# Optimization experiments

Measured on AMD Instinct MI355X. Metric: run time of the kernel, lower is better.

Reference implementation:

```python
import jax, jax.numpy as jnp
import numpy as np

EPS = 1e-4

def mp_weight(w):
    # MP_GeoLinear eval-mode weight: normalize then scale by gain/sqrt(fan_in)
    w32 = w.astype(jnp.float32)
    norm = jnp.linalg.norm(w32, axis=1, keepdims=True)          # [out,1]
    fan_in = w.shape[1]
    denom = EPS + norm / np.sqrt(fan_in)                        # torch.add(eps, norm, alpha=sqrt(1/fan_in))
    wn = w32 / denom
    return (wn / np.sqrt(fan_in)).astype(w.dtype)               # gain=1


def setup_inputs() -> dict:
    key = jax.random.key(0)
    k1, k2, k3, k4 = jax.random.split(key, 4)
    N, E, C = 100000, 1600000, 128
    x = jax.random.normal(k1, (N, C), dtype=jnp.float32)
    edge_index = jax.random.randint(k2, (2, E), 0, N, dtype=jnp.int64)
    w_neigh = jax.random.normal(k3, (C, C), dtype=jnp.float32)
    w_res = jax.random.normal(k4, (C, C), dtype=jnp.float32)
    return {"x": x, "edge_index": edge_index, "w_neigh": w_neigh, "w_res": w_res}


def reference(x, edge_index, w_neigh, w_res):
    N = x.shape[0]
    row, col = edge_index[0], edge_index[1]            # source, target
    # degree of target nodes
    deg = jax.ops.segment_sum(jnp.ones_like(col, dtype=x.dtype), col, num_segments=N)
    deg_inv = jnp.where(deg > 0, deg ** -0.5, 0.0)     # inf -> 0
    norm = deg_inv[col]                                 # [E]
    # message: x_j * norm, aggregate: scatter-add into col
    msg = x[row] * norm[:, None]                        # [E,C]
    agg = jax.ops.segment_sum(msg, col, num_segments=N) # [N,C]
    neighbourhood = agg @ mp_weight(w_neigh).T
    residual = x @ mp_weight(w_res).T
    # mp_sum(residual, neighbourhood, t=0.5) = (a+b)/sqrt(2)
    join = (residual + neighbourhood) / np.sqrt(2.0)
    out = jnp.where((deg > 0)[:, None], join, residual)
    return out
```

## Files before the change

kernel.cpp:

```cpp
#include <hip/hip_runtime.h>
#include <hip/hip_bf16.h>

#define C 128
#define INV_SQRT2 0.7071067811865476f
#define NB 1024
#define BS 128
#define EPB 16384
#define CAPB 2560
#define LIDX_CAP 3456
#define AGS 68
#define GSTRIDE 16

typedef __attribute__((ext_vector_type(8))) short short8;
typedef __attribute__((ext_vector_type(4))) float f32x4;

__device__ inline ushort f2b(float f) {
    __hip_bfloat16 h = __float2bfloat16(f);
    return __builtin_bit_cast(ushort, h);
}


__global__ __launch_bounds__(512) void k_front(
    const int* __restrict__ row, const int* __restrict__ col, int E, int nblk,
    int* __restrict__ gcursor, unsigned int* __restrict__ recs,
    const float4* __restrict__ x, ushort* __restrict__ xb, int n4, int castBlocks,
    const float* __restrict__ w_res, const float* __restrict__ w_neigh,
    ushort* __restrict__ Bp)
{
    __shared__ int hist[NB];
    __shared__ int lbase[NB];
    int b = blockIdx.x;
    int t = threadIdx.x;
    if (b < nblk) {
        hist[t] = 0; hist[t + 512] = 0;
        __syncthreads();
        int base = b * EPB;
        #pragma unroll 4
        for (int i = 0; i < EPB / 512; i++) {
            int e = base + i * 512 + t;
            if (e < E) atomicAdd(&hist[col[e] >> 7], 1);
        }
        __syncthreads();
        #pragma unroll
        for (int kx = 0; kx < 2; kx++) {
            int bb = t + kx * 512;
            int h = hist[bb];
            lbase[bb] = h ? atomicAdd(&gcursor[bb * GSTRIDE], h) : 0;
        }
        __syncthreads();
        hist[t] = 0; hist[t + 512] = 0;
        __syncthreads();
        #pragma unroll 4
        for (int i = 0; i < EPB / 512; i++) {
            int e = base + i * 512 + t;
            if (e < E) {
                int c = col[e];
                int kk = c >> 7;
                int p = atomicAdd(&hist[kk], 1) + lbase[kk];
                if (p < CAPB)
                    recs[(size_t)kk * CAPB + p] =
                        ((unsigned int)(c & 127) << 24) | (unsigned int)row[e];
            }
        }
    } else if (b < nblk + castBlocks) {
        int i = (b - nblk) * 512 + t;
        if (i < n4) {
            float4 v = x[i];
            ushort4 o;
            o.x = f2b(v.x); o.y = f2b(v.y); o.z = f2b(v.z); o.w = f2b(v.w);
            *(ushort4*)(xb + (size_t)i * 4) = o;
        }
        if (b == nblk && t < 32) {
            ushort4 z = make_ushort4(0, 0, 0, 0);
            *(ushort4*)(xb + ((size_t)n4 << 2) + (t << 2)) = z;
        }
    } else {
        int r = (b - nblk - castBlocks) * 8 + (t >> 6);
        int h = r >> 7;
        int i = r & 127;
        const float* w = h ? w_neigh : w_res;
        int lane = t & 63;
        float a = w[i * C + lane];
        float bb = w[i * C + lane + 64];
        float ss = a * a + bb * bb;
        #pragma unroll
        for (int off = 32; off > 0; off >>= 1) ss += __shfl_down(ss, off);
        ss = __shfl(ss, 0);
        float norm = sqrtf(ss);
        float denom = 1e-4f + norm * 0.08838834764831845f;
        float scale = 1.0f / (denom * 11.313708498984761f);
        int c1 = lane, c2 = lane + 64;
        Bp[(size_t)(h * 16 + (c1 >> 3)) * 1024 + i * 8 + (c1 & 7)] = f2b(a * scale);
        Bp[(size_t)(h * 16 + (c2 >> 3)) * 1024 + i * 8 + (c2 & 7)] = f2b(bb * scale);
    }
}


#define ACCUM(v) do { \
    acc[0] += __builtin_bit_cast(float, (v).x << 16); \
    acc[1] += __builtin_bit_cast(float, (v).x & 0xffff0000u); \
    acc[2] += __builtin_bit_cast(float, (v).y << 16); \
    acc[3] += __builtin_bit_cast(float, (v).y & 0xffff0000u); \
    acc[4] += __builtin_bit_cast(float, (v).z << 16); \
    acc[5] += __builtin_bit_cast(float, (v).z & 0xffff0000u); \
    acc[6] += __builtin_bit_cast(float, (v).w << 16); \
    acc[7] += __builtin_bit_cast(float, (v).w & 0xffff0000u); \
} while (0)

__global__ __launch_bounds__(512, 8) void k_fused(
    const unsigned int* __restrict__ recs, const int* __restrict__ gcursor,
    const ushort* __restrict__ xb, const ushort* __restrict__ Bp,
    int* __restrict__ lidxg, float* __restrict__ out, int N)
{
    __shared__ int shist[BS];
    __shared__ int sexcl[BS];
    __shared__ int scur[BS];
    __shared__ uint sAgg[BS * AGS];

    int k = blockIdx.x;
    int t = threadIdx.x;
    int cnt = gcursor[k * GSTRIDE];
    if (cnt > CAPB) cnt = CAPB;
    const unsigned int* rb = recs + (size_t)k * CAPB;
    int* lw = lidxg + (size_t)k * LIDX_CAP;

    if (t < BS) shist[t] = 0;
    __syncthreads();
    for (int i = t; i < cnt; i += 512)
        atomicAdd(&shist[rb[i] >> 24], 1);
    __syncthreads();
    if (t < 64) {
        int a = shist[t], b = shist[t + 64];
        int pa = (a + 7) & ~7, pb = (b + 7) & ~7;
        int ia = pa, ib = pb;
        #pragma unroll
        for (int off = 1; off < 64; off <<= 1) {
            int ya = __shfl_up(ia, off);
            int yb = __shfl_up(ib, off);
            if (t >= off) { ia += ya; ib += yb; }
        }
        int tot0 = __shfl(ia, 63);
        int e0 = ia - pa;
        int e1 = ib - pb + tot0;
        sexcl[t] = e0;      scur[t] = e0;
        sexcl[t + 64] = e1; scur[t + 64] = e1;
    }
    __syncthreads();
    for (int i = t; i < cnt; i += 512) {
        unsigned int r = rb[i];
        int c = r >> 24;
        int p = atomicAdd(&scur[c], 1);
        lw[p] = (int)(r & 0xFFFFFF);
    }
    if (t < BS) {
        int d = shist[t], b0 = sexcl[t];
        int pe = b0 + ((d + 7) & ~7);
        for (int p = b0 + d; p < pe; p++) lw[p] = N;
    }
    __syncthreads();

    int lane = t & 63;
    int wave = t >> 6;
    int s  = lane >> 4;
    int cl = lane & 15;
    const ushort* xcl = xb + (cl << 3);
    #pragma unroll 1
    for (int ln = wave * 16; ln < wave * 16 + 16; ln++) {
        int j  = sexcl[ln];
        int d  = shist[ln];
        int jend = j + ((d + 7) & ~7);
        float acc[8];
        #pragma unroll
        for (int i = 0; i < 8; i++) acc[i] = 0.f;
        for (; j + 16 <= jend; j += 16) {
            int i0 = lw[j + s];
            int i1 = lw[j + 4 + s];
            int i2 = lw[j + 8 + s];
            int i3 = lw[j + 12 + s];
            uint4 va = *(const uint4*)(xcl + ((size_t)i0 << 7));
            uint4 vb = *(const uint4*)(xcl + ((size_t)i1 << 7));
            uint4 vc = *(const uint4*)(xcl + ((size_t)i2 << 7));
            uint4 vd = *(const uint4*)(xcl + ((size_t)i3 << 7));
            ACCUM(va);
            ACCUM(vb);
            ACCUM(vc);
            ACCUM(vd);
        }
        if (j < jend) {
            int i0 = lw[j + s];
            int i1 = lw[j + 4 + s];
            uint4 va = *(const uint4*)(xcl + ((size_t)i0 << 7));
            uint4 vb = *(const uint4*)(xcl + ((size_t)i1 << 7));
            ACCUM(va);
            ACCUM(vb);
        }
        #pragma unroll
        for (int i = 0; i < 8; i++) {
            acc[i] += __shfl_xor(acc[i], 16);
            acc[i] += __shfl_xor(acc[i], 32);
        }
        float dd = (d > 0) ? rsqrtf((float)d) : 0.f;
        if (lane < 16) {
            uint4 o;
            o.x = (uint)f2b(acc[0] * dd) | ((uint)f2b(acc[1] * dd) << 16);
            o.y = (uint)f2b(acc[2] * dd) | ((uint)f2b(acc[3] * dd) << 16);
            o.z = (uint)f2b(acc[4] * dd) | ((uint)f2b(acc[5] * dd) << 16);
            o.w = (uint)f2b(acc[6] * dd) | ((uint)f2b(acc[7] * dd) << 16);
            *(uint4*)&sAgg[ln * AGS + cl * 4] = o;
        }
    }
    asm volatile("s_waitcnt lgkmcnt(0)" ::: "memory");

    int quad = lane >> 4;
    int l16  = lane & 15;
    long gbase = (long)k * BS;
    int arow = wave * 16 + l16;
    long garow = gbase + arow;
    if (garow >= N) garow = N - 1;

    f32x4 oacc[8];
    #pragma unroll
    for (int nt = 0; nt < 8; nt++) oacc[nt] = (f32x4){0.f, 0.f, 0.f, 0.f};

    #pragma unroll
    for (int kk = 0; kk < 8; kk++) {
        short8 af;
        if (kk < 4) {
            af = *(const short8*)(xb + garow * C + kk * 32 + quad * 8);
        } else {
            af = *(const short8*)&sAgg[arow * AGS + (kk - 4) * 16 + quad * 4];
        }
        #pragma unroll
        for (int nt = 0; nt < 8; nt++) {
            short8 bf = *(const short8*)(Bp +
                ((size_t)((kk * 4 + quad) * 128) + nt * 16 + l16) * 8);
            oacc[nt] = __builtin_amdgcn_mfma_f32_16x16x32_bf16(af, bf, oacc[nt], 0, 0, 0);
        }
    }

    #pragma unroll
    for (int r2 = 0; r2 < 4; r2++) {
        int rl = wave * 16 + quad * 4 + r2;
        long rowg = gbase + rl;
        if (rowg < N) {
            float sc = (shist[rl] > 0) ? INV_SQRT2 : 1.0f;
            float* o = out + rowg * C + l16;
            #pragma unroll
            for (int nt = 0; nt < 8; nt++)
                __builtin_nontemporal_store(oacc[nt][r2] * sc, &o[nt * 16]);
        }
    }
}


extern "C" void kernel_launch(void* const* d_in, const int* in_sizes, int n_in,
                              void* d_out, int out_size, void* d_ws, size_t ws_size,
                              hipStream_t stream) {
    const float* x       = (const float*)d_in[0];
    const int*   eidx    = (const int*)d_in[1];
    const float* w_neigh = (const float*)d_in[2];
    const float* w_res   = (const float*)d_in[3];
    float* out = (float*)d_out;

    int N = in_sizes[0] / C;
    int E = in_sizes[1] / 2;
    const int* row = eidx;
    const int* col = eidx + E;

    char* ws = (char*)d_ws;
    size_t off = 0;
    auto alloc = [&](size_t bytes) {
        size_t o = off;
        off += (bytes + 511) & ~(size_t)511;
        return o;
    };
    int nblk = (E + EPB - 1) / EPB;

    int*    gcursor    = (int*)(ws + alloc((size_t)NB * GSTRIDE * 4));
    unsigned int* recs = (unsigned int*)(ws + alloc((size_t)NB * CAPB * 4));
    ushort* Bp         = (ushort*)(ws + alloc((size_t)32 * 1024 * 2));
    ushort* xb         = (ushort*)(ws + alloc((size_t)N * C * 2 + 65536));
    int*    lidxg      = (int*)(ws + alloc((size_t)NB * LIDX_CAP * 4));
    (void)ws_size;

    hipMemsetAsync(gcursor, 0, (size_t)NB * GSTRIDE * 4, stream);

    int nbuckets = (N + BS - 1) / BS;
    int n4 = N * C / 4;
    int castBlocks = (n4 + 511) / 512;

    k_front<<<nblk + castBlocks + 32, 512, 0, stream>>>(
        row, col, E, nblk, gcursor, recs,
        (const float4*)x, xb, n4, castBlocks, w_res, w_neigh, Bp);
    k_fused<<<nbuckets, 512, 0, stream>>>(recs, gcursor, xb, Bp, lidxg, out, N);
}
```

Baseline: 232.6 us.

## Stage bucketed edge records in LDS and write them out coalesced; widen cast blocks

The binning pass now writes each edge record into a shared-memory staging array laid out by bucket, using a wave prefix scan to compute local offsets. It then copies each bucket's contiguous run to global memory with coalesced per-wave stores, instead of scattering individual 4-byte stores across 1024 buckets. The x-to-bf16 cast blocks now each process four float4 elements per thread, which cuts the block count. The cost is 64KB+ of LDS per block, which lowers occupancy for the binning blocks, and a serial per-wave copy loop over the buckets.

```diff
diff --git a/kernel.cpp b/kernel.cpp
--- a/kernel.cpp
+++ b/kernel.cpp
@@ -27,8 +27,11 @@
     const float* __restrict__ w_res, const float* __restrict__ w_neigh,
     ushort* __restrict__ Bp)
 {
+    __shared__ unsigned int srec[EPB];
     __shared__ int hist[NB];
+    __shared__ int lofs[NB];
     __shared__ int lbase[NB];
+    __shared__ int scursor;
     int b = blockIdx.x;
     int t = threadIdx.x;
     if (b < nblk) {
@@ -40,15 +43,28 @@
             int e = base + i * 512 + t;
             if (e < E) atomicAdd(&hist[col[e] >> 7], 1);
         }
+        if (t == 0) scursor = 0;
         __syncthreads();
-        #pragma unroll
-        for (int kx = 0; kx < 2; kx++) {
-            int bb = t + kx * 512;
-            int h = hist[bb];
-            lbase[bb] = h ? atomicAdd(&gcursor[bb * GSTRIDE], h) : 0;
-        }
-        __syncthreads();
-        hist[t] = 0; hist[t + 512] = 0;
+        int k0 = 2 * t, k1 = 2 * t + 1;
+        int h0 = hist[k0], h1 = hist[k1];
+        lbase[k0] = h0 ? atomicAdd(&gcursor[k0 * GSTRIDE], h0) : 0;
+        lbase[k1] = h1 ? atomicAdd(&gcursor[k1 * GSTRIDE], h1) : 0;
+        int lane = t & 63;
+        int hs = h0 + h1;
+        int incl = hs;
+        #pragma unroll
+        for (int off = 1; off < 64; off <<= 1) {
+            int y = __shfl_up(incl, off);
+            if (lane >= off) incl += y;
+        }
+        int wtot = __shfl(incl, 63);
+        int excl = incl - hs;
+        int wbase = 0;
+        if (lane == 63) wbase = atomicAdd(&scursor, wtot);
+        wbase = __shfl(wbase, 63);
+        lofs[k0] = wbase + excl;
+        lofs[k1] = wbase + excl + h0;
+        hist[k0] = 0; hist[k1] = 0;
         __syncthreads();
         #pragma unroll 4
         for (int i = 0; i < EPB / 512; i++) {
@@ -56,19 +72,34 @@
             if (e < E) {
                 int c = col[e];
                 int kk = c >> 7;
-                int p = atomicAdd(&hist[kk], 1) + lbase[kk];
-                if (p < CAPB)
-                    recs[(size_t)kk * CAPB + p] =
-                        ((unsigned int)(c & 127) << 24) | (unsigned int)row[e];
+                int p = atomicAdd(&hist[kk], 1);
+                srec[lofs[kk] + p] =
+                    ((unsigned int)(c & 127) << 24) | (unsigned int)row[e];
             }
         }
+        __syncthreads();
+        int wv = t >> 6;
+        for (int it = 0; it < NB / 8; it++) {
+            int kk = it * 8 + wv;
+            int h = hist[kk];
+            if (h == 0) continue;
+            int gb = lbase[kk];
+            int lo = lofs[kk];
+            int hmax = min(h, CAPB - gb);
+            for (int j = lane; j < hmax; j += 64)
+                recs[(size_t)kk * CAPB + gb + j] = srec[lo + j];
+        }
     } else if (b < nblk + castBlocks) {
-        int i = (b - nblk) * 512 + t;
-        if (i < n4) {
-            float4 v = x[i];
-            ushort4 o;
-            o.x = f2b(v.x); o.y = f2b(v.y); o.z = f2b(v.z); o.w = f2b(v.w);
-            *(ushort4*)(xb + (size_t)i * 4) = o;
+        int i0 = (b - nblk) * 2048 + t;
+        #pragma unroll
+        for (int u = 0; u < 4; u++) {
+            int i = i0 + u * 512;
+            if (i < n4) {
+                float4 v = x[i];
+                ushort4 o;
+                o.x = f2b(v.x); o.y = f2b(v.y); o.z = f2b(v.z); o.w = f2b(v.w);
+                *(ushort4*)(xb + (size_t)i * 4) = o;
+            }
         }
         if (b == nblk && t < 32) {
             ushort4 z = make_ushort4(0, 0, 0, 0);
@@ -287,7 +318,7 @@
 
     int nbuckets = (N + BS - 1) / BS;
     int n4 = N * C / 4;
-    int castBlocks = (n4 + 511) / 512;
+    int castBlocks = (n4 + 2047) / 2048;
 
     k_front<<<nblk + castBlocks + 32, 512, 0, stream>>>(
         row, col, E, nblk, gcursor, recs,
```

Result: slower. 251.3 us (+8.1%).
